# Optimization experiments

Hardware: AMD Instinct MI355X
Metric: run time of the kernel (lower is better)

Reference implementation:

```python
import jax, jax.numpy as jnp
import numpy as np

N, D, H = 96, 64, 256  # num_nodes, input_dim, hidden_dim


def setup_inputs() -> dict:
    key = jax.random.key(0)
    ks = jax.random.split(key, 12)

    def lin(k, fan_in, fan_out):
        return jax.random.normal(k, (fan_in, fan_out), jnp.float32) / np.sqrt(fan_in)

    return {
        "node_features": jax.random.normal(ks[0], (N, D), jnp.float32),
        "edge_index": jax.random.randint(ks[1], (2, 1536), 0, N),
        # causal_discovery MLP: Linear(2D,H) -> ReLU -> Linear(H,H//2) -> ReLU -> Linear(H//2,1) -> Sigmoid
        "W1": lin(ks[2], 2 * D, H),      "b1": jnp.zeros((H,), jnp.float32),
        "W2": lin(ks[3], H, H // 2),     "b2": jnp.zeros((H // 2,), jnp.float32),
        "W3": lin(ks[4], H // 2, 1),     "b3": jnp.zeros((1,), jnp.float32),
        # confounder_detector MLP: Linear(3D,H) -> ReLU -> Linear(H,1) -> Sigmoid
        "V1": lin(ks[5], 3 * D, H),      "c1": jnp.zeros((H,), jnp.float32),
        "V2": lin(ks[6], H, 1),          "c2": jnp.zeros((1,), jnp.float32),
    }


def reference(node_features, edge_index, W1, b1, W2, b2, W3, b3, V1, c1, V2, c2):
    n, d = node_features.shape
    eye = jnp.eye(n, dtype=bool)

    # ---- discover_causal_structure: all ordered pairs (i, j), i != j ----
    # Linear on concat([x_i, x_j]) == x_i @ W1[:d] + x_j @ W1[d:] + b1
    pi = node_features @ W1[:d]           # [N, H]
    pj = node_features @ W1[d:]           # [N, H]
    h = jax.nn.relu(pi[:, None, :] + pj[None, :, :] + b1)   # [N, N, H]
    h = jax.nn.relu(h @ W2 + b2)                             # [N, N, H//2]
    causal = jax.nn.sigmoid((h @ W3 + b3)[..., 0])           # [N, N]
    causal = jnp.where(eye, 0.0, causal)                     # diagonal stays zero

    # ---- detect_confounders: all distinct triplets (i, j, k) ----
    ta = node_features @ V1[:d]            # [N, H]
    tb = node_features @ V1[d:2 * d]       # [N, H]
    tc = node_features @ V1[2 * d:]        # [N, H]
    t = jax.nn.relu(ta[:, None, None, :] + tb[None, :, None, :]
                    + tc[None, None, :, :] + c1)             # [N, N, N, H]
    conf = jax.nn.sigmoid((t @ V2 + c2)[..., 0])             # [N, N, N]
    distinct = (~eye[:, :, None]) & (~eye[None, :, :]) & (~eye[:, None, :])
    conf = jnp.where(distinct, conf, 0.0)

    return causal, conf
```

## Files before the change

### kernel.cpp

```cpp
#include <hip/hip_runtime.h>
#include <hip/hip_bf16.h>

#define NN 96
#define DD 64
#define HH 256
#define H2 128

__global__ __launch_bounds__(256) void proj_kernel(
    const float* __restrict__ X, const float* __restrict__ W1, const float* __restrict__ b1,
    const float* __restrict__ V1, const float* __restrict__ c1,
    float* __restrict__ pi, float* __restrict__ pj,
    float* __restrict__ ta, float* __restrict__ tb, float* __restrict__ tcT)
{
    const int i = blockIdx.x;
    const int h = threadIdx.x;
    __shared__ float xs[DD];
    if (h < DD) xs[h] = X[i*DD + h];
    __syncthreads();
    float aPi = 0.f, aPj = 0.f, aTa = 0.f, aTb = 0.f, aTc = 0.f;
    #pragma unroll 8
    for (int d = 0; d < DD; ++d) {
        const float x = xs[d];
        aPi = fmaf(x, W1[d*HH + h],          aPi);
        aPj = fmaf(x, W1[(DD + d)*HH + h],   aPj);
        aTa = fmaf(x, V1[d*HH + h],          aTa);
        aTb = fmaf(x, V1[(DD + d)*HH + h],   aTb);
        aTc = fmaf(x, V1[(2*DD + d)*HH + h], aTc);
    }
    pi[i*HH + h] = aPi + b1[h];
    pj[i*HH + h] = aPj;
    ta[i*HH + h] = aTa + c1[h];
    tb[i*HH + h] = aTb;
    tcT[h*NN + i] = aTc;
}

__global__ __launch_bounds__(256) void causal_kernel(
    const float* __restrict__ pi, const float* __restrict__ pj,
    const float* __restrict__ W2, const float* __restrict__ b2,
    const float* __restrict__ W3, const float* __restrict__ b3,
    float* __restrict__ out)
{
    const int i  = blockIdx.x;
    const int j0 = blockIdx.y * 12;
    const int t  = threadIdx.x;
    const int c2 = t & 63;
    const int qt = t >> 6;

    __shared__ float smem[4*64*2*12];
    __shared__ float red[2][12];
    float (*hb)[12]          = (float(*)[12])smem;
    float (*part)[64][2][12] = (float(*)[64][2][12])smem;

    {
        const float p_i = pi[i*HH + t];
        #pragma unroll
        for (int jj = 0; jj < 12; ++jj)
            hb[t][jj] = fmaxf(p_i + pj[(j0 + jj)*HH + t], 0.f);
    }
    __syncthreads();

    float acc0[12], acc1[12];
    #pragma unroll
    for (int jj = 0; jj < 12; ++jj) { acc0[jj] = 0.f; acc1[jj] = 0.f; }

    const float* __restrict__ w2p = W2 + (qt*64)*H2 + c2;
    #pragma unroll 2
    for (int q = 0; q < 64; ++q) {
        const float wa = w2p[q*H2];
        const float wb = w2p[q*H2 + 64];
        const int hq = qt*64 + q;
        const float4 hA = *(const float4*)&hb[hq][0];
        const float4 hB = *(const float4*)&hb[hq][4];
        const float4 hC = *(const float4*)&hb[hq][8];
        const float hv[12] = {hA.x,hA.y,hA.z,hA.w, hB.x,hB.y,hB.z,hB.w, hC.x,hC.y,hC.z,hC.w};
        #pragma unroll
        for (int jj = 0; jj < 12; ++jj) {
            acc0[jj] = fmaf(hv[jj], wa, acc0[jj]);
            acc1[jj] = fmaf(hv[jj], wb, acc1[jj]);
        }
    }
    __syncthreads();

    #pragma unroll
    for (int b = 0; b < 3; ++b) {
        float4 p0, p1;
        p0.x = acc0[b*4+0]; p0.y = acc0[b*4+1]; p0.z = acc0[b*4+2]; p0.w = acc0[b*4+3];
        p1.x = acc1[b*4+0]; p1.y = acc1[b*4+1]; p1.z = acc1[b*4+2]; p1.w = acc1[b*4+3];
        *(float4*)&part[qt][c2][0][b*4] = p0;
        *(float4*)&part[qt][c2][1][b*4] = p1;
    }
    __syncthreads();

    if (t < 128) {
        const int c  = t;
        const int cl = t & 63;
        const int cc = t >> 6;
        const float b2c = b2[c];
        const float w3c = W3[c];
        float v[12];
        #pragma unroll
        for (int b = 0; b < 3; ++b) {
            float4 s; s.x = 0.f; s.y = 0.f; s.z = 0.f; s.w = 0.f;
            #pragma unroll
            for (int qq = 0; qq < 4; ++qq) {
                const float4 p = *(const float4*)&part[qq][cl][cc][b*4];
                s.x += p.x; s.y += p.y; s.z += p.z; s.w += p.w;
            }
            v[b*4+0] = fmaxf(s.x + b2c, 0.f) * w3c;
            v[b*4+1] = fmaxf(s.y + b2c, 0.f) * w3c;
            v[b*4+2] = fmaxf(s.z + b2c, 0.f) * w3c;
            v[b*4+3] = fmaxf(s.w + b2c, 0.f) * w3c;
        }
        #pragma unroll
        for (int jj = 0; jj < 12; ++jj) {
            float s = v[jj];
            #pragma unroll
            for (int off = 32; off; off >>= 1) s += __shfl_down(s, off, 64);
            if ((t & 63) == 0) red[t >> 6][jj] = s;
        }
    }
    __syncthreads();
    if (t < 12) {
        const int j = j0 + t;
        const float s = red[0][t] + red[1][t] + b3[0];
        out[i*NN + j] = (i == j) ? 0.f : 1.f / (1.f + __expf(-s));
    }
}

#define CJT 12
#define CJG 3
__global__ __launch_bounds__(192) void conf_kernel(
    const float* __restrict__ ta, const float* __restrict__ tb,
    const float* __restrict__ tcT, const float* __restrict__ V2,
    const float* __restrict__ c2, float* __restrict__ out)
{
    const int i  = blockIdx.x;
    const int j0 = blockIdx.y * CJT;
    const int t  = threadIdx.x;
    const int g  = t / 48;
    const int l  = t % 48;
    const int k0 = 2*l;

    __shared__ float sbuf[CJT][HH];

    for (int idx = t; idx < CJT*HH/4; idx += 192) {
        const int jj = idx >> 6;
        const int h4 = (idx & 63) << 2;
        const float4 a = *(const float4*)&ta[i*HH + h4];
        const float4 b = *(const float4*)&tb[(j0 + jj)*HH + h4];
        float4 s; s.x = a.x + b.x; s.y = a.y + b.y; s.z = a.z + b.z; s.w = a.w + b.w;
        *(float4*)&sbuf[jj][h4] = s;
    }
    __syncthreads();

    float acc[CJG][2];
    #pragma unroll
    for (int m = 0; m < CJG; ++m) { acc[m][0] = 0.f; acc[m][1] = 0.f; }

    const float* __restrict__ sb0 = &sbuf[g*CJG + 0][0];
    const float* __restrict__ sb1 = &sbuf[g*CJG + 1][0];
    const float* __restrict__ sb2 = &sbuf[g*CJG + 2][0];

    #pragma unroll 2
    for (int h0 = 0; h0 < HH; h0 += 4) {
        const float2 t0 = *(const float2*)&tcT[(h0+0)*NN + k0];
        const float2 t1 = *(const float2*)&tcT[(h0+1)*NN + k0];
        const float2 t2 = *(const float2*)&tcT[(h0+2)*NN + k0];
        const float2 t3 = *(const float2*)&tcT[(h0+3)*NN + k0];
        const float4 va = *(const float4*)&V2[h0];
        const float4 sA = *(const float4*)&sb0[h0];
        const float4 sB = *(const float4*)&sb1[h0];
        const float4 sC = *(const float4*)&sb2[h0];
        const float s[CJG][4] = {{sA.x,sA.y,sA.z,sA.w},
                                 {sB.x,sB.y,sB.z,sB.w},
                                 {sC.x,sC.y,sC.z,sC.w}};
        const float tc[4][2] = {{t0.x,t0.y},{t1.x,t1.y},{t2.x,t2.y},{t3.x,t3.y}};
        const float vv[4] = {va.x,va.y,va.z,va.w};
        #pragma unroll
        for (int u4 = 0; u4 < 4; ++u4) {
            #pragma unroll
            for (int m = 0; m < CJG; ++m) {
                acc[m][0] = fmaf(fmaxf(s[m][u4] + tc[u4][0], 0.f), vv[u4], acc[m][0]);
                acc[m][1] = fmaf(fmaxf(s[m][u4] + tc[u4][1], 0.f), vv[u4], acc[m][1]);
            }
        }
    }

    const float c2v = c2[0];
    #pragma unroll
    for (int m = 0; m < CJG; ++m) {
        const int j = j0 + g*CJG + m;
        float2 o;
        o.x = 1.f / (1.f + __expf(-(acc[m][0] + c2v)));
        o.y = 1.f / (1.f + __expf(-(acc[m][1] + c2v)));
        if (i == j || i == k0   || j == k0  ) o.x = 0.f;
        if (i == j || i == k0+1 || j == k0+1) o.y = 0.f;
        *(float2*)&out[(i*NN + j)*NN + k0] = o;
    }
}

extern "C" void kernel_launch(void* const* d_in, const int* in_sizes, int n_in,
                              void* d_out, int out_size, void* d_ws, size_t ws_size,
                              hipStream_t stream) {
    const float* X  = (const float*)d_in[0];
    const float* W1 = (const float*)d_in[2];
    const float* b1 = (const float*)d_in[3];
    const float* W2 = (const float*)d_in[4];
    const float* b2 = (const float*)d_in[5];
    const float* W3 = (const float*)d_in[6];
    const float* b3 = (const float*)d_in[7];
    const float* V1 = (const float*)d_in[8];
    const float* c1 = (const float*)d_in[9];
    const float* V2 = (const float*)d_in[10];
    const float* c2 = (const float*)d_in[11];

    float* out = (float*)d_out;
    float* ws  = (float*)d_ws;
    float* pi  = ws;
    float* pj  = pi + NN*HH;
    float* ta  = pj + NN*HH;
    float* tb  = ta + NN*HH;
    float* tcT = tb + NN*HH;

    proj_kernel<<<NN, 256, 0, stream>>>(X, W1, b1, V1, c1, pi, pj, ta, tb, tcT);
    causal_kernel<<<dim3(NN, 8), 256, 0, stream>>>(pi, pj, W2, b2, W3, b3, out);
    conf_kernel<<<dim3(NN, 8), 192, 0, stream>>>(ta, tb, tcT, V2, c2, out + NN*NN);
}
```

Baseline: 48.84 us.

## Split projection across five matrices and software-pipeline loads in causal/conf loops

The projection kernel is split so each block computes one of the five projections, giving five times more blocks on a small grid. The causal kernel's W2 loop is unrolled into chunks of 8 with register double-buffering of the next chunk's weights. The conf kernel's loop prefetches the next iteration's tcT, V2 and shared-memory operands before computing the current one. The aim is to hide global/LDS latency and fill more CUs, at the cost of more registers and redundant X loads per block.

```diff
diff --git a/kernel.cpp b/kernel.cpp
--- a/kernel.cpp
+++ b/kernel.cpp
@@ -13,25 +13,28 @@
     float* __restrict__ ta, float* __restrict__ tb, float* __restrict__ tcT)
 {
     const int i = blockIdx.x;
+    const int m = blockIdx.y;
     const int h = threadIdx.x;
     __shared__ float xs[DD];
     if (h < DD) xs[h] = X[i*DD + h];
     __syncthreads();
-    float aPi = 0.f, aPj = 0.f, aTa = 0.f, aTb = 0.f, aTc = 0.f;
-    #pragma unroll 8
-    for (int d = 0; d < DD; ++d) {
-        const float x = xs[d];
-        aPi = fmaf(x, W1[d*HH + h],          aPi);
-        aPj = fmaf(x, W1[(DD + d)*HH + h],   aPj);
-        aTa = fmaf(x, V1[d*HH + h],          aTa);
-        aTb = fmaf(x, V1[(DD + d)*HH + h],   aTb);
-        aTc = fmaf(x, V1[(2*DD + d)*HH + h], aTc);
-    }
-    pi[i*HH + h] = aPi + b1[h];
-    pj[i*HH + h] = aPj;
-    ta[i*HH + h] = aTa + c1[h];
-    tb[i*HH + h] = aTb;
-    tcT[h*NN + i] = aTc;
+
+    const float* __restrict__ W =
+        (m == 0) ? W1 :
+        (m == 1) ? W1 + DD*HH :
+        (m == 2) ? V1 :
+        (m == 3) ? V1 + DD*HH : V1 + 2*DD*HH;
+
+    float acc = 0.f;
+    #pragma unroll 16
+    for (int d = 0; d < DD; ++d)
+        acc = fmaf(xs[d], W[d*HH + h], acc);
+
+    if      (m == 0) pi[i*HH + h] = acc + b1[h];
+    else if (m == 1) pj[i*HH + h] = acc;
+    else if (m == 2) ta[i*HH + h] = acc + c1[h];
+    else if (m == 3) tb[i*HH + h] = acc;
+    else             tcT[h*NN + i] = acc;
 }
 
 __global__ __launch_bounds__(256) void causal_kernel(
@@ -64,20 +67,33 @@
     for (int jj = 0; jj < 12; ++jj) { acc0[jj] = 0.f; acc1[jj] = 0.f; }
 
     const float* __restrict__ w2p = W2 + (qt*64)*H2 + c2;
-    #pragma unroll 2
-    for (int q = 0; q < 64; ++q) {
-        const float wa = w2p[q*H2];
-        const float wb = w2p[q*H2 + 64];
-        const int hq = qt*64 + q;
-        const float4 hA = *(const float4*)&hb[hq][0];
-        const float4 hB = *(const float4*)&hb[hq][4];
-        const float4 hC = *(const float4*)&hb[hq][8];
-        const float hv[12] = {hA.x,hA.y,hA.z,hA.w, hB.x,hB.y,hB.z,hB.w, hC.x,hC.y,hC.z,hC.w};
-        #pragma unroll
-        for (int jj = 0; jj < 12; ++jj) {
-            acc0[jj] = fmaf(hv[jj], wa, acc0[jj]);
-            acc1[jj] = fmaf(hv[jj], wb, acc1[jj]);
-        }
+
+    float wa[8], wb[8];
+    #pragma unroll
+    for (int u = 0; u < 8; ++u) { wa[u] = w2p[u*H2]; wb[u] = w2p[u*H2 + 64]; }
+
+    #pragma unroll
+    for (int cch = 0; cch < 8; ++cch) {
+        float xa[8], xb[8];
+        const int nq = (cch < 7) ? (cch + 1)*8 : 0;
+        #pragma unroll
+        for (int u = 0; u < 8; ++u) { xa[u] = w2p[(nq + u)*H2]; xb[u] = w2p[(nq + u)*H2 + 64]; }
+
+        #pragma unroll
+        for (int u = 0; u < 8; ++u) {
+            const int hq = qt*64 + cch*8 + u;
+            const float4 hA = *(const float4*)&hb[hq][0];
+            const float4 hB = *(const float4*)&hb[hq][4];
+            const float4 hC = *(const float4*)&hb[hq][8];
+            const float hv[12] = {hA.x,hA.y,hA.z,hA.w, hB.x,hB.y,hB.z,hB.w, hC.x,hC.y,hC.z,hC.w};
+            #pragma unroll
+            for (int jj = 0; jj < 12; ++jj) {
+                acc0[jj] = fmaf(hv[jj], wa[u], acc0[jj]);
+                acc1[jj] = fmaf(hv[jj], wb[u], acc1[jj]);
+            }
+        }
+        #pragma unroll
+        for (int u = 0; u < 8; ++u) { wa[u] = xa[u]; wb[u] = xb[u]; }
     }
     __syncthreads();
 
@@ -161,21 +177,31 @@
     const float* __restrict__ sb1 = &sbuf[g*CJG + 1][0];
     const float* __restrict__ sb2 = &sbuf[g*CJG + 2][0];
 
+#define LOADC(H0, T, VA, S)                                 \
+    T[0] = *(const float2*)&tcT[((H0)+0)*NN + k0];          \
+    T[1] = *(const float2*)&tcT[((H0)+1)*NN + k0];          \
+    T[2] = *(const float2*)&tcT[((H0)+2)*NN + k0];          \
+    T[3] = *(const float2*)&tcT[((H0)+3)*NN + k0];          \
+    VA   = *(const float4*)&V2[(H0)];                       \
+    S[0] = *(const float4*)&sb0[(H0)];                      \
+    S[1] = *(const float4*)&sb1[(H0)];                      \
+    S[2] = *(const float4*)&sb2[(H0)];
+
+    float2 ct[4]; float4 cva; float4 cs[CJG];
+    LOADC(0, ct, cva, cs);
+
     #pragma unroll 2
     for (int h0 = 0; h0 < HH; h0 += 4) {
-        const float2 t0 = *(const float2*)&tcT[(h0+0)*NN + k0];
-        const float2 t1 = *(const float2*)&tcT[(h0+1)*NN + k0];
-        const float2 t2 = *(const float2*)&tcT[(h0+2)*NN + k0];
-        const float2 t3 = *(const float2*)&tcT[(h0+3)*NN + k0];
-        const float4 va = *(const float4*)&V2[h0];
-        const float4 sA = *(const float4*)&sb0[h0];
-        const float4 sB = *(const float4*)&sb1[h0];
-        const float4 sC = *(const float4*)&sb2[h0];
-        const float s[CJG][4] = {{sA.x,sA.y,sA.z,sA.w},
-                                 {sB.x,sB.y,sB.z,sB.w},
-                                 {sC.x,sC.y,sC.z,sC.w}};
-        const float tc[4][2] = {{t0.x,t0.y},{t1.x,t1.y},{t2.x,t2.y},{t3.x,t3.y}};
-        const float vv[4] = {va.x,va.y,va.z,va.w};
+        float2 nt[4]; float4 nva; float4 ns[CJG];
+        const int hn = (h0 + 4) & (HH - 1);
+        LOADC(hn, nt, nva, ns);
+
+        const float vv[4] = {cva.x, cva.y, cva.z, cva.w};
+        const float s[CJG][4] = {{cs[0].x,cs[0].y,cs[0].z,cs[0].w},
+                                 {cs[1].x,cs[1].y,cs[1].z,cs[1].w},
+                                 {cs[2].x,cs[2].y,cs[2].z,cs[2].w}};
+        const float tc[4][2] = {{ct[0].x,ct[0].y},{ct[1].x,ct[1].y},
+                                {ct[2].x,ct[2].y},{ct[3].x,ct[3].y}};
         #pragma unroll
         for (int u4 = 0; u4 < 4; ++u4) {
             #pragma unroll
@@ -184,7 +210,11 @@
                 acc[m][1] = fmaf(fmaxf(s[m][u4] + tc[u4][1], 0.f), vv[u4], acc[m][1]);
             }
         }
-    }
+        ct[0] = nt[0]; ct[1] = nt[1]; ct[2] = nt[2]; ct[3] = nt[3];
+        cva = nva;
+        cs[0] = ns[0]; cs[1] = ns[1]; cs[2] = ns[2];
+    }
+#undef LOADC
 
     const float c2v = c2[0];
     #pragma unroll
@@ -222,7 +252,7 @@
     float* tb  = ta + NN*HH;
     float* tcT = tb + NN*HH;
 
-    proj_kernel<<<NN, 256, 0, stream>>>(X, W1, b1, V1, c1, pi, pj, ta, tb, tcT);
+    proj_kernel<<<dim3(NN, 5), 256, 0, stream>>>(X, W1, b1, V1, c1, pi, pj, ta, tb, tcT);
     causal_kernel<<<dim3(NN, 8), 256, 0, stream>>>(pi, pj, W2, b2, W3, b3, out);
     conf_kernel<<<dim3(NN, 8), 192, 0, stream>>>(ta, tb, tcT, V2, c2, out + NN*NN);
 }
```

New measurement: 52.45 us. +7.4%, slower.

## Split conf_kernel hidden dim across lane pairs with 4-wide k tiles

Applied to the files above, without the earlier changes.

The confounder kernel now gives each thread 4 consecutive k values and half of the hidden dimension, instead of 2 k values over the full hidden dimension. Partial sums are combined with a lane-pair shuffle, and only even lanes write float4 outputs. Each loaded tc/sbuf value is reused across more outputs and the loop runs half as many iterations per thread. The shared buffer row is padded to 260 floats to reduce LDS bank conflicts between the two half-rows. In exchange, each thread holds more accumulator registers, and half the threads sit idle during the output stage.

```diff
diff --git a/kernel.cpp b/kernel.cpp
--- a/kernel.cpp
+++ b/kernel.cpp
@@ -127,23 +127,24 @@
     }
 }
 
-#define CJT 12
-#define CJG 3
+#define CROW 260
 __global__ __launch_bounds__(192) void conf_kernel(
     const float* __restrict__ ta, const float* __restrict__ tb,
     const float* __restrict__ tcT, const float* __restrict__ V2,
     const float* __restrict__ c2, float* __restrict__ out)
 {
     const int i  = blockIdx.x;
-    const int j0 = blockIdx.y * CJT;
+    const int j0 = blockIdx.y * 12;
     const int t  = threadIdx.x;
-    const int g  = t / 48;
+    const int jg = t / 48;
     const int l  = t % 48;
-    const int k0 = 2*l;
-
-    __shared__ float sbuf[CJT][HH];
-
-    for (int idx = t; idx < CJT*HH/4; idx += 192) {
+    const int kp = l >> 1;
+    const int hh = l & 1;
+    const int k0 = kp * 4;
+
+    __shared__ float sbuf[12][CROW];
+
+    for (int idx = t; idx < 12*64; idx += 192) {
         const int jj = idx >> 6;
         const int h4 = (idx & 63) << 2;
         const float4 a = *(const float4*)&ta[i*HH + h4];
@@ -153,49 +154,70 @@
     }
     __syncthreads();
 
-    float acc[CJG][2];
-    #pragma unroll
-    for (int m = 0; m < CJG; ++m) { acc[m][0] = 0.f; acc[m][1] = 0.f; }
-
-    const float* __restrict__ sb0 = &sbuf[g*CJG + 0][0];
-    const float* __restrict__ sb1 = &sbuf[g*CJG + 1][0];
-    const float* __restrict__ sb2 = &sbuf[g*CJG + 2][0];
+    float acc[3][4];
+    #pragma unroll
+    for (int m = 0; m < 3; ++m)
+        #pragma unroll
+        for (int x = 0; x < 4; ++x) acc[m][x] = 0.f;
+
+    const int hbase = hh << 7;
+    const float* __restrict__ sb0 = &sbuf[jg*3 + 0][hbase];
+    const float* __restrict__ sb1 = &sbuf[jg*3 + 1][hbase];
+    const float* __restrict__ sb2 = &sbuf[jg*3 + 2][hbase];
+    const float* __restrict__ tp  = tcT + hbase*NN + k0;
+    const float* __restrict__ vp  = V2 + hbase;
 
     #pragma unroll 2
-    for (int h0 = 0; h0 < HH; h0 += 4) {
-        const float2 t0 = *(const float2*)&tcT[(h0+0)*NN + k0];
-        const float2 t1 = *(const float2*)&tcT[(h0+1)*NN + k0];
-        const float2 t2 = *(const float2*)&tcT[(h0+2)*NN + k0];
-        const float2 t3 = *(const float2*)&tcT[(h0+3)*NN + k0];
-        const float4 va = *(const float4*)&V2[h0];
-        const float4 sA = *(const float4*)&sb0[h0];
-        const float4 sB = *(const float4*)&sb1[h0];
-        const float4 sC = *(const float4*)&sb2[h0];
-        const float s[CJG][4] = {{sA.x,sA.y,sA.z,sA.w},
-                                 {sB.x,sB.y,sB.z,sB.w},
-                                 {sC.x,sC.y,sC.z,sC.w}};
-        const float tc[4][2] = {{t0.x,t0.y},{t1.x,t1.y},{t2.x,t2.y},{t3.x,t3.y}};
-        const float vv[4] = {va.x,va.y,va.z,va.w};
-        #pragma unroll
-        for (int u4 = 0; u4 < 4; ++u4) {
+    for (int hq = 0; hq < 128; hq += 4) {
+        const float4 t0 = *(const float4*)&tp[(hq+0)*NN];
+        const float4 t1 = *(const float4*)&tp[(hq+1)*NN];
+        const float4 t2 = *(const float4*)&tp[(hq+2)*NN];
+        const float4 t3 = *(const float4*)&tp[(hq+3)*NN];
+        const float4 vv = *(const float4*)&vp[hq];
+        const float4 sA = *(const float4*)&sb0[hq];
+        const float4 sB = *(const float4*)&sb1[hq];
+        const float4 sC = *(const float4*)&sb2[hq];
+        const float sm[3][4] = {{sA.x,sA.y,sA.z,sA.w},
+                                {sB.x,sB.y,sB.z,sB.w},
+                                {sC.x,sC.y,sC.z,sC.w}};
+        const float tk[4][4] = {{t0.x,t0.y,t0.z,t0.w},
+                                {t1.x,t1.y,t1.z,t1.w},
+                                {t2.x,t2.y,t2.z,t2.w},
+                                {t3.x,t3.y,t3.z,t3.w}};
+        const float vvv[4] = {vv.x, vv.y, vv.z, vv.w};
+        #pragma unroll
+        for (int u = 0; u < 4; ++u)
             #pragma unroll
-            for (int m = 0; m < CJG; ++m) {
-                acc[m][0] = fmaf(fmaxf(s[m][u4] + tc[u4][0], 0.f), vv[u4], acc[m][0]);
-                acc[m][1] = fmaf(fmaxf(s[m][u4] + tc[u4][1], 0.f), vv[u4], acc[m][1]);
+            for (int m = 0; m < 3; ++m) {
+                acc[m][0] = fmaf(fmaxf(sm[m][u] + tk[u][0], 0.f), vvv[u], acc[m][0]);
+                acc[m][1] = fmaf(fmaxf(sm[m][u] + tk[u][1], 0.f), vvv[u], acc[m][1]);
+                acc[m][2] = fmaf(fmaxf(sm[m][u] + tk[u][2], 0.f), vvv[u], acc[m][2]);
+                acc[m][3] = fmaf(fmaxf(sm[m][u] + tk[u][3], 0.f), vvv[u], acc[m][3]);
             }
-        }
-    }
-
-    const float c2v = c2[0];
-    #pragma unroll
-    for (int m = 0; m < CJG; ++m) {
-        const int j = j0 + g*CJG + m;
-        float2 o;
-        o.x = 1.f / (1.f + __expf(-(acc[m][0] + c2v)));
-        o.y = 1.f / (1.f + __expf(-(acc[m][1] + c2v)));
-        if (i == j || i == k0   || j == k0  ) o.x = 0.f;
-        if (i == j || i == k0+1 || j == k0+1) o.y = 0.f;
-        *(float2*)&out[(i*NN + j)*NN + k0] = o;
+    }
+
+    #pragma unroll
+    for (int m = 0; m < 3; ++m)
+        #pragma unroll
+        for (int x = 0; x < 4; ++x)
+            acc[m][x] += __shfl_xor(acc[m][x], 1, 64);
+
+    if (hh == 0) {
+        const float c2v = c2[0];
+        #pragma unroll
+        for (int m = 0; m < 3; ++m) {
+            const int j = j0 + jg*3 + m;
+            float4 o;
+            o.x = 1.f / (1.f + __expf(-(acc[m][0] + c2v)));
+            o.y = 1.f / (1.f + __expf(-(acc[m][1] + c2v)));
+            o.z = 1.f / (1.f + __expf(-(acc[m][2] + c2v)));
+            o.w = 1.f / (1.f + __expf(-(acc[m][3] + c2v)));
+            if (i == j || i == k0   || j == k0  ) o.x = 0.f;
+            if (i == j || i == k0+1 || j == k0+1) o.y = 0.f;
+            if (i == j || i == k0+2 || j == k0+2) o.z = 0.f;
+            if (i == j || i == k0+3 || j == k0+3) o.w = 0.f;
+            *(float4*)&out[(i*NN + j)*NN + k0] = o;
+        }
     }
 }
 
```

Result: slower. 49.92 us (+2.2%).
